# Kernel tuning notes

Measured on AMD Instinct MI355X. Metric: run time of the kernel, lower is better.

Reference implementation:

```python
import jax, jax.numpy as jnp
import numpy as np

INF = 1.0e6  # 'infinity' for squared EDT; max real value is ~3*128^2 ~ 5e4


def edt_1d_sq(f, axis):
    """One pass of Felzenszwalb separable squared EDT along `axis`.
    d[i] = min_j f[j] + (i - j)^2  (brute-force vectorized lower envelope)."""
    f = jnp.moveaxis(f, axis, -1)
    n = f.shape[-1]
    i = jnp.arange(n, dtype=f.dtype)
    sq = (i[:, None] - i[None, :]) ** 2  # (n, n)
    d = jnp.min(f[..., None, :] + sq, axis=-1)  # (..., n)
    return jnp.moveaxis(d, -1, axis)


def compute_fg_dtm(mask):
    """Euclidean distance transform of foreground (distance to nearest background),
    matching scipy.ndimage.distance_transform_edt applied per batch element on the
    (C, X, Y, Z) mask (C==1 so the channel axis pass is the identity).
    mask: bool (B, 1, X, Y, Z) -> float32 (B, 1, X, Y, Z)."""
    def per_b(m):
        g = jnp.where(m, jnp.float32(INF), jnp.float32(0.0))
        for ax in range(m.ndim):
            g = edt_1d_sq(g, ax)
        return jnp.sqrt(g)
    return jax.lax.map(per_b, mask)


def setup_inputs() -> dict:
    key = jax.random.key(0)
    k1, k2, k3 = jax.random.split(key, 3)
    B, C, X, Y, Z = 2, 2, 128, 128, 128
    return {
        "outputs": jax.random.normal(k1, (B, C, X, Y, Z), dtype=jnp.float32),
        "outputs_dist": jax.random.normal(k2, (B, C, X, Y, Z), dtype=jnp.float32) * 10.0,
        "y": jax.random.randint(k3, (B, 1, X, Y, Z), 0, 2),
        "distance_map_weight": 1.0,
    }


def reference(outputs, outputs_dist, y, distance_map_weight):
    n_pred_ch = outputs.shape[1]
    # MONAI one_hot: (B,1,X,Y,Z) int labels -> (B,C,X,Y,Z) float
    y1h = jnp.moveaxis(jax.nn.one_hot(y[:, 0], n_pred_ch, dtype=outputs.dtype), -1, 1)
    x = outputs[:, 1:]            # foreground logits (B, 1, X, Y, Z)
    t = y1h[:, 1:]                # foreground mask
    od = outputs_dist[:, 1:]
    gt_dis = compute_fg_dtm(t > 0.5)
    # BCE with logits (mean reduction), numerically stable
    loss_ce = jnp.mean(jnp.maximum(x, 0.0) - x * t + jnp.log1p(jnp.exp(-jnp.abs(x))))
    # dice loss, flattened per batch element
    N = x.shape[0]
    smooth = jnp.float32(1.0)
    p = jax.nn.sigmoid(x).reshape(N, -1)
    tf = t.reshape(N, -1)
    dice = (2.0 * jnp.sum(p * tf, axis=1) + smooth) / (jnp.sum(p, axis=1) + jnp.sum(tf, axis=1) + smooth)
    loss_dice = 1.0 - jnp.sum(dice) / N
    # weighted L1 on the distance head, masked by the foreground mask
    msum = jnp.sum(t)
    loss_dist = jnp.where(
        msum == 0,
        jnp.float32(0.0),
        jnp.sum(jnp.abs(od - gt_dis) * t) / jnp.maximum(msum, jnp.float32(1e-12)),
    )
    return loss_ce + loss_dice + distance_map_weight * loss_dist
```

## Files before the change

### kernel.cpp

```cpp
#include <hip/hip_runtime.h>
#include <math.h>

#define M_SPATIAL 2097152

__device__ __forceinline__ float wave_redf(float v) {
#pragma unroll
  for (int o = 32; o > 0; o >>= 1) v += __shfl_down(v, o, 64);
  return v;
}
__device__ __forceinline__ double wave_redd(double v) {
#pragma unroll
  for (int o = 32; o > 0; o >>= 1) v += __shfl_down(v, o, 64);
  return v;
}
__device__ __forceinline__ float min3f(float a, float b, float c) {
  float d;
  asm("v_min3_f32 %0, %1, %2, %3" : "=v"(d) : "v"(a), "v"(b), "v"(c));
  return d;
}


__global__ __launch_bounds__(256) void kAB(const int* __restrict__ y,
                                           const float* __restrict__ outputs,
                                           float* __restrict__ g,
                                           double* __restrict__ part) {
  int blk = blockIdx.x;
  int b  = blk >> 9;
  int yy = (blk >> 2) & 127;
  int zq = blk & 3;
  int t  = threadIdx.x;
  int c  = t >> 5;
  int zl = t & 31;
  int x0 = c * 16;
  size_t sp   = (size_t)yy * 128 + (size_t)zq * 32 + zl;
  size_t base = (size_t)b * M_SPATIAL + sp;
  const float* xc = outputs + (size_t)(b * 2 + 1) * M_SPATIAL;

  int yb[16];
  float xv[16];
#pragma unroll
  for (int k = 0; k < 16; ++k) yb[k] = y[base + (size_t)(x0 + k) * 16384];
#pragma unroll
  for (int k = 0; k < 16; ++k) xv[k] = xc[sp + (size_t)(x0 + k) * 16384];

  int lastE = -200, nextE = 400;
#pragma unroll
  for (int k = 0; k < 16; ++k) lastE = (yb[k] == 1) ? lastE : (x0 + k);
#pragma unroll
  for (int k = 15; k >= 0; --k) nextE = (yb[k] == 1) ? nextE : (x0 + k);

  __shared__ int lE[8][32];
  __shared__ int nE[8][32];
  lE[c][zl] = lastE;
  nE[c][zl] = nextE;
  __syncthreads();

  int carryL = -200, carryN = 400;
#pragma unroll
  for (int q = 0; q < 7; ++q) {
    if (q < c)     carryL = max(carryL, lE[q][zl]);
    if (q + 1 > c) carryN = min(carryN, nE[q + 1][zl]);
  }

  float yy2f = (float)(yy * yy);
  float hinf = 1000000.f + yy2f;

  int df[16];
  int ll = carryL;
#pragma unroll
  for (int k = 0; k < 16; ++k) {
    ll = (yb[k] == 1) ? ll : (x0 + k);
    df[k] = min(x0 + k - ll, 200);
  }
  float ov[16];
  int nn = carryN;
#pragma unroll
  for (int k = 15; k >= 0; --k) {
    nn = (yb[k] == 1) ? nn : (x0 + k);
    int m = min(df[k], min(nn - (x0 + k), 200));
    ov[k] = (m >= 128) ? hinf : ((float)(m * m) + yy2f);
  }
#pragma unroll
  for (int k = 0; k < 16; ++k) g[base + (size_t)(x0 + k) * 16384] = ov[k];

  float ce = 0.f, ps = 0.f, pts = 0.f, tsum = 0.f;
#pragma unroll
  for (int k = 0; k < 16; ++k) {
    float tt = (yb[k] == 1) ? 1.0f : 0.0f;
    float xx = xv[k];
    ce += fmaxf(xx, 0.0f) - xx * tt + log1pf(expf(-fabsf(xx)));
    float p = 1.0f / (1.0f + expf(-xx));
    ps += p; pts += p * tt; tsum += tt;
  }
  float r0 = wave_redf(ce), r1 = wave_redf(ps), r2 = wave_redf(pts), r3 = wave_redf(tsum);
  __shared__ float sm[4][4];
  int lane = t & 63, w = t >> 6;
  if (lane == 0) { sm[w][0] = r0; sm[w][1] = r1; sm[w][2] = r2; sm[w][3] = r3; }
  __syncthreads();
  if (t == 0) {
    part[blk]        = (double)(sm[0][0] + sm[1][0] + sm[2][0] + sm[3][0]);
    part[1024 + blk] = (double)(sm[0][1] + sm[1][1] + sm[2][1] + sm[3][1]);
    part[2048 + blk] = (double)(sm[0][2] + sm[1][2] + sm[2][2] + sm[3][2]);
    part[3072 + blk] = (double)(sm[0][3] + sm[1][3] + sm[2][3] + sm[3][3]);
  }
}

__global__ __launch_bounds__(256) void kC_edty(float* __restrict__ g) {
  __shared__ float hl[144 * 33];
  int blk = blockIdx.x;
  int b = blk >> 9, xx = (blk >> 2) & 127, zc = blk & 3;
  int t = threadIdx.x;
  size_t rb = (size_t)b * M_SPATIAL + (size_t)xx * 16384 + (size_t)zc * 32;

#pragma unroll
  for (int idx = t; idx < 264; idx += 256) {
    hl[idx] = 1.0e9f;
    hl[136 * 33 + idx] = 1.0e9f;
  }
#pragma unroll
  for (int r = 0; r < 4; ++r) {
    int i4 = t + r * 256;
    int j = i4 >> 3, w = i4 & 7;
    float4 v = *(const float4*)(g + rb + (size_t)j * 128 + 4 * w);
    hl[(j + 8) * 33 + 4 * w + 0] = v.x;
    hl[(j + 8) * 33 + 4 * w + 1] = v.y;
    hl[(j + 8) * 33 + 4 * w + 2] = v.z;
    hl[(j + 8) * 33 + 4 * w + 3] = v.w;
  }
  __syncthreads();

  int zl = t & 31, ig = t >> 5;
  int ibase = ig * 16;
  float best[16], mc[16];
#pragma unroll
  for (int k = 0; k < 16; ++k) {
    best[k] = 3.0e38f;
    mc[k] = -2.0f * (float)(ibase + k);
  }
  float jb = (float)(ibase - 8);
#pragma unroll 4
  for (int p = 0; p < 16; ++p) {
    float h0 = hl[(ibase + 2 * p) * 33 + zl];
    float h1 = hl[(ibase + 2 * p + 1) * 33 + zl];
    float j0 = jb + (float)(2 * p), j1 = jb + (float)(2 * p + 1);
#pragma unroll
    for (int k = 0; k < 16; ++k) {
      float v0 = fmaf(mc[k], j0, h0);
      float v1 = fmaf(mc[k], j1, h1);
      best[k] = min3f(v0, v1, best[k]);
    }
  }
  float dv[16];
  int ok = 1;
#pragma unroll
  for (int k = 0; k < 16; ++k) {
    int i = ibase + k;
    dv[k] = (float)(i * i) + best[k];
    float bnd = (float)min((k + 9) * (k + 9), (24 - k) * (24 - k));
    ok &= (dv[k] <= bnd);
  }
  if (!__all(ok)) {
#pragma unroll
    for (int k = 0; k < 16; ++k) best[k] = 3.0e38f;
#pragma unroll 2
    for (int j = 0; j < 128; j += 2) {
      float h0 = hl[(j + 8) * 33 + zl];
      float h1 = hl[(j + 9) * 33 + zl];
      float j0 = (float)j, j1 = (float)(j + 1);
#pragma unroll
      for (int k = 0; k < 16; ++k) {
        float v0 = fmaf(mc[k], j0, h0);
        float v1 = fmaf(mc[k], j1, h1);
        best[k] = min3f(v0, v1, best[k]);
      }
    }
#pragma unroll
    for (int k = 0; k < 16; ++k) {
      int i = ibase + k;
      dv[k] = (float)(i * i) + best[k];
    }
  }
  int gz = zc * 32 + zl;
  float zq = (float)(gz * gz);
  size_t ob = rb + zl;
#pragma unroll
  for (int k = 0; k < 16; ++k) {
    int i = ibase + k;
    g[ob + (size_t)i * 128] = dv[k] + zq;
  }
}

__global__ __launch_bounds__(256) void kD_edtz_dist(const float* __restrict__ g,
                                                    const float* __restrict__ od,
                                                    double* __restrict__ part) {
  __shared__ float hl[144 * 33];
  __shared__ float sred[4];
  int blk = blockIdx.x;
  int b = blk >> 9, xx = (blk >> 2) & 127, yc = blk & 3;
  int t = threadIdx.x;
  size_t rb = (size_t)b * M_SPATIAL + (size_t)xx * 16384 + (size_t)yc * 4096;
  int yl = t & 31, ig = t >> 5;
  int ibase = ig * 16;

  size_t odb = (size_t)(2 * b + 1) * M_SPATIAL + (size_t)xx * 16384 +
               (size_t)yc * 4096 + (size_t)yl * 128 + (size_t)ibase;
  const float4* o4 = (const float4*)(od + odb);
  float4 ov[4];
#pragma unroll
  for (int r = 0; r < 4; ++r) ov[r] = o4[r];

#pragma unroll
  for (int idx = t; idx < 264; idx += 256) {
    hl[idx] = 1.0e9f;
    hl[136 * 33 + idx] = 1.0e9f;
  }
  const float4* h4 = (const float4*)(g + rb);
#pragma unroll
  for (int r = 0; r < 4; ++r) {
    int i4 = t + r * 256;
    float4 v = h4[i4];
    int flat = i4 * 4;
    int z = flat & 127, yw = flat >> 7;
    hl[(z + 8) * 33 + yw] = v.x;
    hl[(z + 9) * 33 + yw] = v.y;
    hl[(z + 10) * 33 + yw] = v.z;
    hl[(z + 11) * 33 + yw] = v.w;
  }
  __syncthreads();

  float best[16], mc[16];
#pragma unroll
  for (int k = 0; k < 16; ++k) {
    best[k] = 3.0e38f;
    mc[k] = -2.0f * (float)(ibase + k);
  }
  float jb = (float)(ibase - 8);
#pragma unroll 4
  for (int p = 0; p < 16; ++p) {
    float h0 = hl[(ibase + 2 * p) * 33 + yl];
    float h1 = hl[(ibase + 2 * p + 1) * 33 + yl];
    float j0 = jb + (float)(2 * p), j1 = jb + (float)(2 * p + 1);
#pragma unroll
    for (int k = 0; k < 16; ++k) {
      float v0 = fmaf(mc[k], j0, h0);
      float v1 = fmaf(mc[k], j1, h1);
      best[k] = min3f(v0, v1, best[k]);
    }
  }
  float dv[16];
  int ok = 1;
#pragma unroll
  for (int k = 0; k < 16; ++k) {
    int i = ibase + k;
    dv[k] = (float)(i * i) + best[k];
    float bnd = (float)min((k + 9) * (k + 9), (24 - k) * (24 - k));
    ok &= (dv[k] <= bnd);
  }
  if (!__all(ok)) {
#pragma unroll
    for (int k = 0; k < 16; ++k) best[k] = 3.0e38f;
#pragma unroll 2
    for (int j = 0; j < 128; j += 2) {
      float h0 = hl[(j + 8) * 33 + yl];
      float h1 = hl[(j + 9) * 33 + yl];
      float j0 = (float)j, j1 = (float)(j + 1);
#pragma unroll
      for (int k = 0; k < 16; ++k) {
        float v0 = fmaf(mc[k], j0, h0);
        float v1 = fmaf(mc[k], j1, h1);
        best[k] = min3f(v0, v1, best[k]);
      }
    }
#pragma unroll
    for (int k = 0; k < 16; ++k) {
      int i = ibase + k;
      dv[k] = (float)(i * i) + best[k];
    }
  }
  const float* of = (const float*)ov;
  float dist = 0.f;
#pragma unroll
  for (int k = 0; k < 16; ++k) {
    if (dv[k] > 0.f) dist += fabsf(of[k] - sqrtf(dv[k]));
  }
  float r = wave_redf(dist);
  int lane = t & 63, w = t >> 6;
  if (lane == 0) sred[w] = r;
  __syncthreads();
  if (t == 0) part[4096 + blk] = (double)(sred[0] + sred[1] + sred[2] + sred[3]);
}

__global__ __launch_bounds__(256) void k_final(const double* __restrict__ part,
                                               const float* __restrict__ wptr,
                                               float* __restrict__ out) {
  int i = threadIdx.x;
  double ce  = part[i] + part[i + 256] + part[i + 512] + part[i + 768];
  double p0  = part[1024 + i] + part[1024 + i + 256];
  double p1  = part[1536 + i] + part[1536 + i + 256];
  double pt0 = part[2048 + i] + part[2048 + i + 256];
  double pt1 = part[2560 + i] + part[2560 + i + 256];
  double t0  = part[3072 + i] + part[3072 + i + 256];
  double t1  = part[3584 + i] + part[3584 + i + 256];
  double ds  = part[4096 + i] + part[4096 + i + 256] + part[4096 + i + 512] + part[4096 + i + 768];

  ce = wave_redd(ce); p0 = wave_redd(p0); p1 = wave_redd(p1);
  pt0 = wave_redd(pt0); pt1 = wave_redd(pt1);
  t0 = wave_redd(t0); t1 = wave_redd(t1); ds = wave_redd(ds);

  __shared__ double sm[4][8];
  int lane = threadIdx.x & 63, w = threadIdx.x >> 6;
  if (lane == 0) {
    sm[w][0] = ce; sm[w][1] = p0; sm[w][2] = p1; sm[w][3] = pt0;
    sm[w][4] = pt1; sm[w][5] = t0; sm[w][6] = t1; sm[w][7] = ds;
  }
  __syncthreads();
  if (threadIdx.x == 0) {
    double a[8];
    for (int q = 0; q < 8; ++q) a[q] = sm[0][q] + sm[1][q] + sm[2][q] + sm[3][q];
    double cem = a[0] / 4194304.0;
    double dice0 = (2.0 * a[3] + 1.0) / (a[1] + a[5] + 1.0);
    double dice1 = (2.0 * a[4] + 1.0) / (a[2] + a[6] + 1.0);
    double ldice = 1.0 - 0.5 * (dice0 + dice1);
    double msum = a[5] + a[6];
    double ldist = (msum == 0.0) ? 0.0 : a[7] / fmax(msum, 1e-12);
    out[0] = (float)(cem + ldice + (double)wptr[0] * ldist);
  }
}

extern "C" void kernel_launch(void* const* d_in, const int* in_sizes, int n_in,
                              void* d_out, int out_size, void* d_ws, size_t ws_size,
                              hipStream_t stream) {
  const float* outputs      = (const float*)d_in[0];
  const float* outputs_dist = (const float*)d_in[1];
  const int*   y            = (const int*)d_in[2];
  const float* wptr         = (const float*)d_in[3];
  float* out = (float*)d_out;

  double* part = (double*)d_ws;
  float* g = (float*)((char*)d_ws + 65536);

  kAB<<<1024, 256, 0, stream>>>(y, outputs, g, part);
  kC_edty<<<1024, 256, 0, stream>>>(g);
  kD_edtz_dist<<<1024, 256, 0, stream>>>(g, outputs_dist, part);
  k_final<<<1, 256, 0, stream>>>(part, wptr, out);
}
```

Before: 141.9 us.

## Fuse Y and Z EDT passes into one kernel with whole-slab shared memory

Merges the Y-axis EDT kernel and the Z-axis EDT plus distance-loss kernel into a single kernel. Each block now loads a full 128x128 slab into LDS, runs the Y pass, transposes the result back into LDS, then runs the Z pass and the L1 reduction. This removes one global write and one global read of the 2M-element intermediate per batch element, plus one kernel launch. In exchange it drops to 256 blocks of 512 threads with about 74KB of LDS each, so occupancy is roughly one block per CU, which reduces latency hiding.

```diff
diff --git a/kernel.cpp b/kernel.cpp
--- a/kernel.cpp
+++ b/kernel.cpp
@@ -105,68 +105,48 @@
   }
 }
 
-__global__ __launch_bounds__(256) void kC_edty(float* __restrict__ g) {
-  __shared__ float hl[144 * 33];
+__global__ __launch_bounds__(512, 1) void kCD(const float* __restrict__ g,
+                                              const float* __restrict__ od,
+                                              double* __restrict__ part) {
+  __shared__ float hl[144 * 129];
+  __shared__ float sred[8];
   int blk = blockIdx.x;
-  int b = blk >> 9, xx = (blk >> 2) & 127, zc = blk & 3;
+  int b = blk >> 7, xx = blk & 127;
   int t = threadIdx.x;
-  size_t rb = (size_t)b * M_SPATIAL + (size_t)xx * 16384 + (size_t)zc * 32;
-
-#pragma unroll
-  for (int idx = t; idx < 264; idx += 256) {
+  size_t rb = (size_t)b * M_SPATIAL + (size_t)xx * 16384;
+
+  for (int idx = t; idx < 8 * 129; idx += 512) {
     hl[idx] = 1.0e9f;
-    hl[136 * 33 + idx] = 1.0e9f;
-  }
-#pragma unroll
-  for (int r = 0; r < 4; ++r) {
-    int i4 = t + r * 256;
-    int j = i4 >> 3, w = i4 & 7;
-    float4 v = *(const float4*)(g + rb + (size_t)j * 128 + 4 * w);
-    hl[(j + 8) * 33 + 4 * w + 0] = v.x;
-    hl[(j + 8) * 33 + 4 * w + 1] = v.y;
-    hl[(j + 8) * 33 + 4 * w + 2] = v.z;
-    hl[(j + 8) * 33 + 4 * w + 3] = v.w;
-  }
-  __syncthreads();
-
-  int zl = t & 31, ig = t >> 5;
-  int ibase = ig * 16;
-  float best[16], mc[16];
-#pragma unroll
-  for (int k = 0; k < 16; ++k) {
-    best[k] = 3.0e38f;
-    mc[k] = -2.0f * (float)(ibase + k);
-  }
-  float jb = (float)(ibase - 8);
+    hl[136 * 129 + idx] = 1.0e9f;
+  }
+  const float4* g4 = (const float4*)(g + rb);
+#pragma unroll
+  for (int r = 0; r < 8; ++r) {
+    int i4 = t + r * 512;
+    float4 v = g4[i4];
+    int yy = i4 >> 5, z4 = (i4 & 31) * 4;
+    float* p = &hl[(yy + 8) * 129 + z4];
+    p[0] = v.x; p[1] = v.y; p[2] = v.z; p[3] = v.w;
+  }
+  __syncthreads();
+
+  int zcol = t & 127, ig = t >> 7;
+  float dvy[2][16];
+#pragma unroll
+  for (int cb = 0; cb < 2; ++cb) {
+    int ibase = ig * 32 + cb * 16;
+    float best[16], mc[16];
+#pragma unroll
+    for (int k = 0; k < 16; ++k) {
+      best[k] = 3.0e38f;
+      mc[k] = -2.0f * (float)(ibase + k);
+    }
+    float jb = (float)(ibase - 8);
 #pragma unroll 4
-  for (int p = 0; p < 16; ++p) {
-    float h0 = hl[(ibase + 2 * p) * 33 + zl];
-    float h1 = hl[(ibase + 2 * p + 1) * 33 + zl];
-    float j0 = jb + (float)(2 * p), j1 = jb + (float)(2 * p + 1);
-#pragma unroll
-    for (int k = 0; k < 16; ++k) {
-      float v0 = fmaf(mc[k], j0, h0);
-      float v1 = fmaf(mc[k], j1, h1);
-      best[k] = min3f(v0, v1, best[k]);
-    }
-  }
-  float dv[16];
-  int ok = 1;
-#pragma unroll
-  for (int k = 0; k < 16; ++k) {
-    int i = ibase + k;
-    dv[k] = (float)(i * i) + best[k];
-    float bnd = (float)min((k + 9) * (k + 9), (24 - k) * (24 - k));
-    ok &= (dv[k] <= bnd);
-  }
-  if (!__all(ok)) {
-#pragma unroll
-    for (int k = 0; k < 16; ++k) best[k] = 3.0e38f;
-#pragma unroll 2
-    for (int j = 0; j < 128; j += 2) {
-      float h0 = hl[(j + 8) * 33 + zl];
-      float h1 = hl[(j + 9) * 33 + zl];
-      float j0 = (float)j, j1 = (float)(j + 1);
+    for (int p = 0; p < 16; ++p) {
+      float h0 = hl[(ibase + 2 * p) * 129 + zcol];
+      float h1 = hl[(ibase + 2 * p + 1) * 129 + zcol];
+      float j0 = jb + (float)(2 * p), j1 = jb + (float)(2 * p + 1);
 #pragma unroll
       for (int k = 0; k < 16; ++k) {
         float v0 = fmaf(mc[k], j0, h0);
@@ -174,96 +154,74 @@
         best[k] = min3f(v0, v1, best[k]);
       }
     }
+    int ok = 1;
 #pragma unroll
     for (int k = 0; k < 16; ++k) {
       int i = ibase + k;
-      dv[k] = (float)(i * i) + best[k];
-    }
-  }
-  int gz = zc * 32 + zl;
-  float zq = (float)(gz * gz);
-  size_t ob = rb + zl;
-#pragma unroll
-  for (int k = 0; k < 16; ++k) {
-    int i = ibase + k;
-    g[ob + (size_t)i * 128] = dv[k] + zq;
-  }
-}
-
-__global__ __launch_bounds__(256) void kD_edtz_dist(const float* __restrict__ g,
-                                                    const float* __restrict__ od,
-                                                    double* __restrict__ part) {
-  __shared__ float hl[144 * 33];
-  __shared__ float sred[4];
-  int blk = blockIdx.x;
-  int b = blk >> 9, xx = (blk >> 2) & 127, yc = blk & 3;
-  int t = threadIdx.x;
-  size_t rb = (size_t)b * M_SPATIAL + (size_t)xx * 16384 + (size_t)yc * 4096;
-  int yl = t & 31, ig = t >> 5;
-  int ibase = ig * 16;
-
+      dvy[cb][k] = (float)(i * i) + best[k];
+      float bnd = (float)min((k + 9) * (k + 9), (24 - k) * (24 - k));
+      ok &= (dvy[cb][k] <= bnd);
+    }
+    if (!__all(ok)) {
+#pragma unroll
+      for (int k = 0; k < 16; ++k) best[k] = 3.0e38f;
+#pragma unroll 2
+      for (int j = 0; j < 128; j += 2) {
+        float h0 = hl[(j + 8) * 129 + zcol];
+        float h1 = hl[(j + 9) * 129 + zcol];
+        float j0 = (float)j, j1 = (float)(j + 1);
+#pragma unroll
+        for (int k = 0; k < 16; ++k) {
+          float v0 = fmaf(mc[k], j0, h0);
+          float v1 = fmaf(mc[k], j1, h1);
+          best[k] = min3f(v0, v1, best[k]);
+        }
+      }
+#pragma unroll
+      for (int k = 0; k < 16; ++k) {
+        int i = ibase + k;
+        dvy[cb][k] = (float)(i * i) + best[k];
+      }
+    }
+  }
+  __syncthreads();
+  {
+    float zq = (float)(zcol * zcol);
+#pragma unroll
+    for (int cb = 0; cb < 2; ++cb) {
+      int ibase = ig * 32 + cb * 16;
+#pragma unroll
+      for (int k = 0; k < 16; ++k)
+        hl[(zcol + 8) * 129 + (ibase + k)] = dvy[cb][k] + zq;
+    }
+  }
+  __syncthreads();
+
+  int ycol = t & 127, izg = t >> 7;
   size_t odb = (size_t)(2 * b + 1) * M_SPATIAL + (size_t)xx * 16384 +
-               (size_t)yc * 4096 + (size_t)yl * 128 + (size_t)ibase;
+               (size_t)ycol * 128 + (size_t)izg * 32;
   const float4* o4 = (const float4*)(od + odb);
-  float4 ov[4];
-#pragma unroll
-  for (int r = 0; r < 4; ++r) ov[r] = o4[r];
-
-#pragma unroll
-  for (int idx = t; idx < 264; idx += 256) {
-    hl[idx] = 1.0e9f;
-    hl[136 * 33 + idx] = 1.0e9f;
-  }
-  const float4* h4 = (const float4*)(g + rb);
-#pragma unroll
-  for (int r = 0; r < 4; ++r) {
-    int i4 = t + r * 256;
-    float4 v = h4[i4];
-    int flat = i4 * 4;
-    int z = flat & 127, yw = flat >> 7;
-    hl[(z + 8) * 33 + yw] = v.x;
-    hl[(z + 9) * 33 + yw] = v.y;
-    hl[(z + 10) * 33 + yw] = v.z;
-    hl[(z + 11) * 33 + yw] = v.w;
-  }
-  __syncthreads();
-
-  float best[16], mc[16];
-#pragma unroll
-  for (int k = 0; k < 16; ++k) {
-    best[k] = 3.0e38f;
-    mc[k] = -2.0f * (float)(ibase + k);
-  }
-  float jb = (float)(ibase - 8);
+  float4 ovv[8];
+#pragma unroll
+  for (int r = 0; r < 8; ++r) ovv[r] = o4[r];
+  const float* of = (const float*)ovv;
+
+  float dist = 0.f;
+#pragma unroll
+  for (int cb = 0; cb < 2; ++cb) {
+    int izb = izg * 32 + cb * 16;
+    float best[16], mc[16];
+#pragma unroll
+    for (int k = 0; k < 16; ++k) {
+      best[k] = 3.0e38f;
+      mc[k] = -2.0f * (float)(izb + k);
+    }
+    float jb = (float)(izb - 8);
 #pragma unroll 4
-  for (int p = 0; p < 16; ++p) {
-    float h0 = hl[(ibase + 2 * p) * 33 + yl];
-    float h1 = hl[(ibase + 2 * p + 1) * 33 + yl];
-    float j0 = jb + (float)(2 * p), j1 = jb + (float)(2 * p + 1);
-#pragma unroll
-    for (int k = 0; k < 16; ++k) {
-      float v0 = fmaf(mc[k], j0, h0);
-      float v1 = fmaf(mc[k], j1, h1);
-      best[k] = min3f(v0, v1, best[k]);
-    }
-  }
-  float dv[16];
-  int ok = 1;
-#pragma unroll
-  for (int k = 0; k < 16; ++k) {
-    int i = ibase + k;
-    dv[k] = (float)(i * i) + best[k];
-    float bnd = (float)min((k + 9) * (k + 9), (24 - k) * (24 - k));
-    ok &= (dv[k] <= bnd);
-  }
-  if (!__all(ok)) {
-#pragma unroll
-    for (int k = 0; k < 16; ++k) best[k] = 3.0e38f;
-#pragma unroll 2
-    for (int j = 0; j < 128; j += 2) {
-      float h0 = hl[(j + 8) * 33 + yl];
-      float h1 = hl[(j + 9) * 33 + yl];
-      float j0 = (float)j, j1 = (float)(j + 1);
+    for (int p = 0; p < 16; ++p) {
+      float h0 = hl[(izb + 2 * p) * 129 + ycol];
+      float h1 = hl[(izb + 2 * p + 1) * 129 + ycol];
+      float j0 = jb + (float)(2 * p), j1 = jb + (float)(2 * p + 1);
 #pragma unroll
       for (int k = 0; k < 16; ++k) {
         float v0 = fmaf(mc[k], j0, h0);
@@ -271,23 +229,51 @@
         best[k] = min3f(v0, v1, best[k]);
       }
     }
-#pragma unroll
-    for (int k = 0; k < 16; ++k) {
-      int i = ibase + k;
+    float dv[16];
+    int ok = 1;
+#pragma unroll
+    for (int k = 0; k < 16; ++k) {
+      int i = izb + k;
       dv[k] = (float)(i * i) + best[k];
-    }
-  }
-  const float* of = (const float*)ov;
-  float dist = 0.f;
-#pragma unroll
-  for (int k = 0; k < 16; ++k) {
-    if (dv[k] > 0.f) dist += fabsf(of[k] - sqrtf(dv[k]));
+      float bnd = (float)min((k + 9) * (k + 9), (24 - k) * (24 - k));
+      ok &= (dv[k] <= bnd);
+    }
+    if (!__all(ok)) {
+#pragma unroll
+      for (int k = 0; k < 16; ++k) best[k] = 3.0e38f;
+#pragma unroll 2
+      for (int j = 0; j < 128; j += 2) {
+        float h0 = hl[(j + 8) * 129 + ycol];
+        float h1 = hl[(j + 9) * 129 + ycol];
+        float j0 = (float)j, j1 = (float)(j + 1);
+#pragma unroll
+        for (int k = 0; k < 16; ++k) {
+          float v0 = fmaf(mc[k], j0, h0);
+          float v1 = fmaf(mc[k], j1, h1);
+          best[k] = min3f(v0, v1, best[k]);
+        }
+      }
+#pragma unroll
+      for (int k = 0; k < 16; ++k) {
+        int i = izb + k;
+        dv[k] = (float)(i * i) + best[k];
+      }
+    }
+#pragma unroll
+    for (int k = 0; k < 16; ++k) {
+      if (dv[k] > 0.f) dist += fabsf(of[cb * 16 + k] - sqrtf(dv[k]));
+    }
   }
   float r = wave_redf(dist);
   int lane = t & 63, w = t >> 6;
   if (lane == 0) sred[w] = r;
   __syncthreads();
-  if (t == 0) part[4096 + blk] = (double)(sred[0] + sred[1] + sred[2] + sred[3]);
+  if (t == 0) {
+    float s = 0.f;
+#pragma unroll
+    for (int q = 0; q < 8; ++q) s += sred[q];
+    part[4096 + blk] = (double)s;
+  }
 }
 
 __global__ __launch_bounds__(256) void k_final(const double* __restrict__ part,
@@ -301,7 +287,7 @@
   double pt1 = part[2560 + i] + part[2560 + i + 256];
   double t0  = part[3072 + i] + part[3072 + i + 256];
   double t1  = part[3584 + i] + part[3584 + i + 256];
-  double ds  = part[4096 + i] + part[4096 + i + 256] + part[4096 + i + 512] + part[4096 + i + 768];
+  double ds  = part[4096 + i];
 
   ce = wave_redd(ce); p0 = wave_redd(p0); p1 = wave_redd(p1);
   pt0 = wave_redd(pt0); pt1 = wave_redd(pt1);
@@ -340,7 +326,6 @@
   float* g = (float*)((char*)d_ws + 65536);
 
   kAB<<<1024, 256, 0, stream>>>(y, outputs, g, part);
-  kC_edty<<<1024, 256, 0, stream>>>(g);
-  kD_edtz_dist<<<1024, 256, 0, stream>>>(g, outputs_dist, part);
+  kCD<<<256, 512, 0, stream>>>(g, outputs_dist, part);
   k_final<<<1, 256, 0, stream>>>(part, wptr, out);
 }
```

After: 139.1 us (median of 2 runs). 2.0% less time.
